# Kernel optimization log

Hardware: AMD Instinct MI355X
Metric: run time of the kernel (lower is better)

The kernel has to match this reference:

```python
import jax, jax.numpy as jnp
import numpy as np

B, S, D = 4, 2048, 512
H, DK, DV = 8, 64, 64

def setup_inputs() -> dict:
    key = jax.random.key(0)
    ks = jax.random.split(key, 11)
    s = 0.02
    return {
        "q_in": jax.random.normal(ks[0], (B, S, D), jnp.float32),
        "k_in": jax.random.normal(ks[1], (B, S, D), jnp.float32),
        "v_in": jax.random.normal(ks[2], (B, S, D), jnp.float32),
        "Wq": jax.random.normal(ks[3], (H, D, DK), jnp.float32) * s,
        "bq": jax.random.normal(ks[4], (H, DK), jnp.float32) * s,
        "Wk": jax.random.normal(ks[5], (H, D, DK), jnp.float32) * s,
        "bk": jax.random.normal(ks[6], (H, DK), jnp.float32) * s,
        "Wv": jax.random.normal(ks[7], (H, D, DV), jnp.float32) * s,
        "bv": jax.random.normal(ks[8], (H, DV), jnp.float32) * s,
        "Wo": jax.random.normal(ks[9], (H * DV, D), jnp.float32) * s,
        "bo": jax.random.normal(ks[10], (D,), jnp.float32) * s,
    }


def reference(q_in, k_in, v_in, Wq, bq, Wk, bk, Wv, bv, Wo, bo):
    # Per-head Q/K/V projections, batched over heads (same math as the
    # original Python loop over SingleAttention heads).
    q = jnp.einsum("bsd,hdk->bhsk", q_in, Wq) + bq[None, :, None, :]   # [B,H,S,DK]
    k = jnp.einsum("bsd,hdk->bhsk", k_in, Wk) + bk[None, :, None, :]   # [B,H,S,DK]
    v = jnp.einsum("bsd,hdv->bhsv", v_in, Wv) + bv[None, :, None, :]   # [B,H,S,DV]
    scale = 1.0 / jnp.sqrt(jnp.float32(DK))
    scores = jnp.einsum("bhqk,bhsk->bhqs", q, k) * scale               # [B,H,S,S]
    attn = jax.nn.softmax(scores, axis=-1)
    out = jnp.einsum("bhqs,bhsv->bhqv", attn, v)                        # [B,H,S,DV]
    # concat heads along feature dim: [B,S,H*DV]
    concat = out.transpose(0, 2, 1, 3).reshape(B, S, H * DV)
    return concat @ Wo + bo                                             # [B,S,D]
```

## Files before the change

### kernel.cpp

```cpp
#include <hip/hip_runtime.h>
#include <hip/hip_bf16.h>

using bf16 = __hip_bfloat16;
typedef short short8  __attribute__((ext_vector_type(8)));
typedef short short4v __attribute__((ext_vector_type(4)));
typedef float float4v __attribute__((ext_vector_type(4)));
typedef float f32x16  __attribute__((ext_vector_type(16)));
typedef unsigned int uint4v __attribute__((ext_vector_type(4)));

#define MFMA_BF16   __builtin_amdgcn_mfma_f32_16x16x32_bf16
#define MFMA32_BF16 __builtin_amdgcn_mfma_f32_32x32x16_bf16

#define B_  4
#define S_  2048
#define D_  512
#define H_  8
#define DK_ 64

__device__ __forceinline__ short f2bf(float f) {
  bf16 h = __float2bfloat16(f);
  return *reinterpret_cast<short*>(&h);
}

__device__ __forceinline__ unsigned cvtpk(float lo, float hi) {
  unsigned r;
  asm("v_cvt_pk_bf16_f32 %0, %1, %2" : "=v"(r) : "v"(lo), "v"(hi));
  return r;
}

__device__ __forceinline__ void plswap(unsigned& a, unsigned& b) {
  asm("v_permlane32_swap_b32 %0, %1" : "+v"(a), "+v"(b));
}

__device__ __forceinline__ short8 mk8(unsigned v0, unsigned v1, unsigned v2,
                                      unsigned v3) {
  uint4v u;
  u[0] = v0; u[1] = v1; u[2] = v2; u[3] = v3;
  return __builtin_bit_cast(short8, u);
}

#define GLL(g, l) __builtin_amdgcn_global_load_lds(                        \
      (const __attribute__((address_space(1))) void*)(g),                  \
      (__attribute__((address_space(3))) void*)(l), 16, 0, 0)

__global__ __launch_bounds__(256)
void prep(const float* __restrict__ qin, const float* __restrict__ kin,
          const float* __restrict__ vin, short* __restrict__ Xb,
          const float* __restrict__ Wq, const float* __restrict__ Wk,
          const float* __restrict__ Wv, const float* __restrict__ Wo,
          short* __restrict__ WqT, short* __restrict__ WkT,
          short* __restrict__ WvT, short* __restrict__ WoT) {
  __shared__ float tile[64 * 65];
  const int bid = blockIdx.x, tid = threadIdx.x;
  const size_t NTOK = (size_t)B_ * S_ * D_;

  if (bid < 6144) {
    const int z = bid >> 11, blk = bid & 2047;
    const float* src = (z == 0) ? qin : (z == 1) ? kin : vin;
    short* dst = Xb + (size_t)z * NTOK;
    const size_t base = ((size_t)blk * 256 + tid) * 8;
    float4v f0 = *(const float4v*)&src[base];
    float4v f1 = *(const float4v*)&src[base + 4];
    short8 s;
#pragma unroll
    for (int j = 0; j < 4; j++) { s[j] = f2bf(f0[j]); s[j + 4] = f2bf(f1[j]); }
    *(short8*)&dst[base] = s;
    return;
  }

  const int tw = bid - 6144;
  const int mat = tw >> 6, t = tw & 63;
  const float* W = (mat == 0) ? Wq : (mat == 1) ? Wk : (mat == 2) ? Wv : Wo;
  short* T       = (mat == 0) ? WqT : (mat == 1) ? WkT : (mat == 2) ? WvT : WoT;

  size_t sbase, ss, dbase;
  if (mat < 3) {
    int hh = t >> 3, d0 = (t & 7) * 64;
    sbase = (size_t)hh * 32768 + (size_t)d0 * 64;
    ss = 64;
    dbase = (size_t)hh * 64 * 512 + d0;
  } else {
    int n0 = (t >> 3) * 64, k0 = (t & 7) * 64;
    sbase = (size_t)k0 * 512 + n0;
    ss = 512;
    dbase = (size_t)n0 * 512 + k0;
  }

  {
    int r = tid >> 2, c0 = (tid & 3) * 16;
#pragma unroll
    for (int j = 0; j < 4; j++)
      *(float4v*)&tile[r * 65 + c0 + j * 4] =
          *(const float4v*)&W[sbase + (size_t)r * ss + c0 + j * 4];
  }
  __syncthreads();
  {
    int c = tid >> 2, r0 = (tid & 3) * 16;
#pragma unroll
    for (int j = 0; j < 2; j++) {
      short8 s;
#pragma unroll
      for (int u = 0; u < 8; u++) s[u] = f2bf(tile[(r0 + j * 8 + u) * 65 + c]);
      *(short8*)&T[dbase + (size_t)c * 512 + r0 + j * 8] = s;
    }
  }
}

__device__ __forceinline__ void gemm_core2(const short* __restrict__ A,
                                           const short* __restrict__ Bt,
                                           int m0, int n0,
                                           short* As, short* Bs,
                                           float4v acc[4][4]) {
  const int tid  = threadIdx.x;
  const int lane = tid & 63, wave = tid >> 6;
  const int quad = lane >> 4, l16 = lane & 15;
  const int wm = (wave >> 1) * 64, wn = (wave & 1) * 64;

  const int slot = wave * 256 + lane;

  for (int k0 = 0; k0 < 512; k0 += 64) {
    __syncthreads();
#pragma unroll
    for (int i = 0; i < 4; i++) {
      int s = slot + i * 64;
      int row = s >> 3, c8 = (s & 7) * 8;
      GLL(&A[(size_t)(m0 + row) * 512 + k0 + c8],
          &As[(size_t)(wave * 256 + i * 64) * 8]);
      GLL(&Bt[(size_t)(n0 + row) * 512 + k0 + c8],
          &Bs[(size_t)(wave * 256 + i * 64) * 8]);
    }
    __syncthreads();
#pragma unroll
    for (int ks = 0; ks < 64; ks += 32) {
      short8 af[4], bfr[4];
#pragma unroll
      for (int mi = 0; mi < 4; mi++)
        af[mi] = *(short8*)&As[(wm + mi * 16 + l16) * 64 + ks + quad * 8];
#pragma unroll
      for (int ni = 0; ni < 4; ni++)
        bfr[ni] = *(short8*)&Bs[(wn + ni * 16 + l16) * 64 + ks + quad * 8];
#pragma unroll
      for (int mi = 0; mi < 4; mi++)
#pragma unroll
        for (int ni = 0; ni < 4; ni++)
          acc[mi][ni] = MFMA_BF16(af[mi], bfr[ni], acc[mi][ni], 0, 0, 0);
    }
  }
}

__global__ __launch_bounds__(256, 2)
void qkv_gemm(const short* __restrict__ Xb,
              const short* __restrict__ WqT, const short* __restrict__ WkT,
              const short* __restrict__ WvT,
              const float* __restrict__ bq, const float* __restrict__ bk,
              const float* __restrict__ bv,
              short* __restrict__ Qp, short* __restrict__ Kp,
              short* __restrict__ Vt) {
  __shared__ __align__(16) short As[128 * 64];
  __shared__ __align__(16) short Bs[128 * 64];
  const int m0 = blockIdx.x * 128, n0 = blockIdx.y * 128;
  const int z = blockIdx.z;
  const size_t NTOK = (size_t)B_ * S_ * D_;
  const short* A    = Xb + (size_t)z * NTOK;
  const short* Bt   = (z == 0) ? WqT : (z == 1) ? WkT : WvT;
  const float* bias = (z == 0) ? bq  : (z == 1) ? bk  : bv;
  const float scale = (z == 0) ? 0.125f * 1.44269504088896f : 1.0f;

  float4v acc[4][4];
#pragma unroll
  for (int mi = 0; mi < 4; mi++)
#pragma unroll
    for (int ni = 0; ni < 4; ni++) acc[mi][ni] = (float4v){0.f, 0.f, 0.f, 0.f};

  gemm_core2(A, Bt, m0, n0, As, Bs, acc);

  const int lane = threadIdx.x & 63, wave = threadIdx.x >> 6;
  const int quad = lane >> 4, l16 = lane & 15;
  const int wm = (wave >> 1) * 64, wn = (wave & 1) * 64;

  if (z < 2) {
    short* out = (z == 0) ? Qp : Kp;
#pragma unroll
    for (int mi = 0; mi < 4; mi++) {
      int m = m0 + wm + mi * 16 + quad * 4;
      int b = m >> 11, s = m & 2047;
#pragma unroll
      for (int ni = 0; ni < 4; ni++) {
        int n = n0 + wn + ni * 16 + l16;
        int h = n >> 6, dk = n & 63;
        float bb = bias[n];
        size_t base = (((size_t)b * H_ + h) * S_ + s) * 64 + dk;
#pragma unroll
        for (int r = 0; r < 4; r++)
          out[base + (size_t)r * 64] = f2bf((acc[mi][ni][r] + bb) * scale);
      }
    }
  } else {
#pragma unroll
    for (int mi = 0; mi < 4; mi++) {
      int m = m0 + wm + mi * 16 + quad * 4;
      int b = m >> 11, s = m & 2047;
#pragma unroll
      for (int ni = 0; ni < 4; ni++) {
        int n = n0 + wn + ni * 16 + l16;
        int h = n >> 6, v = n & 63;
        float bb = bias[n];
        short4v pk;
#pragma unroll
        for (int r = 0; r < 4; r++) pk[r] = f2bf(acc[mi][ni][r] + bb);
        *(short4v*)&Vt[(((size_t)b * H_ + h) * 64 + v) * S_ + s] = pk;
      }
    }
  }
}

__global__ __launch_bounds__(256, 4)
void attn_kernel(const short* __restrict__ Qp, const short* __restrict__ Kp,
                 const short* __restrict__ Vt, short* __restrict__ Ao) {
  __shared__ __align__(16) short Ksh[2][4096];
  __shared__ __align__(16) short Vsh[2][4096];

  const int orig = blockIdx.y * gridDim.x + blockIdx.x;
  const int lb = (orig & 7) * 64 + (orig >> 3);
  const int qt = lb & 15, bh = lb >> 4;
  const int b = bh >> 3, h = bh & 7;

  const int tid = threadIdx.x;
  const int lane = tid & 63, wave = tid >> 6;
  const int l31 = lane & 31, hi = lane >> 5, s7 = l31 & 7;

  const short* Qb = Qp + (size_t)bh * S_ * 64;
  const short* Kb = Kp + (size_t)bh * S_ * 64;
  const short* Vb = Vt + (size_t)bh * 64 * S_;

  short8 qf[4];
  {
    const short* qrow = Qb + (size_t)(qt * 128 + wave * 32 + l31) * 64;
#pragma unroll
    for (int w = 0; w < 4; w++)
      qf[w] = *(const short8*)&qrow[w * 16 + hi * 8];
  }

  const int slot0 = wave * 128 + lane;
  const int kr0 = slot0 >> 3, kc0 = slot0 & 7;
  const int kr1 = kr0 + 8;
  const short* kg0 = Kb + (size_t)kr0 * 64 + ((kc0 ^ (kr0 & 7)) << 3);
  const short* kg1 = Kb + (size_t)kr1 * 64 + ((kc0 ^ (kr1 & 7)) << 3);
  const short* vg0 = Vb + (size_t)kr0 * S_ + ((kc0 ^ (kr0 & 7)) << 3);
  const short* vg1 = Vb + (size_t)kr1 * S_ + ((kc0 ^ (kr1 & 7)) << 3);

  f32x16 acc0, acc1;
#pragma unroll
  for (int r = 0; r < 16; r++) { acc0[r] = 0.f; acc1[r] = 0.f; }
  float ls0 = 0.f, ls1 = 0.f;

  {
    short* kd = &Ksh[0][wave * 1024];
    short* vd = &Vsh[0][wave * 1024];
    GLL(kg0, kd); GLL(kg1, kd + 512);
    GLL(vg0, vd); GLL(vg1, vd + 512);
  }
  __syncthreads();

  for (int t = 0; t < 32; t++) {
    const int cur = t & 1;
    if (t < 31) {
      short* kd = &Ksh[cur ^ 1][wave * 1024];
      short* vd = &Vsh[cur ^ 1][wave * 1024];
      GLL(kg0 + (size_t)(t + 1) * 4096, kd);
      GLL(kg1 + (size_t)(t + 1) * 4096, kd + 512);
      GLL(vg0 + (size_t)(t + 1) * 64, vd);
      GLL(vg1 + (size_t)(t + 1) * 64, vd + 512);
    }
    const short* kb = Ksh[cur];
    const short* vs = Vsh[cur];

#pragma unroll
    for (int kt = 0; kt < 2; kt++) {
      f32x16 sa;
#pragma unroll
      for (int r = 0; r < 16; r++) sa[r] = 0.f;
      __builtin_amdgcn_s_setprio(1);
#pragma unroll
      for (int w = 0; w < 4; w++) {
        short8 kf = *(const short8*)&kb[(kt * 32 + l31) * 64 +
                                        (((2 * w + hi) ^ s7) << 3)];
        sa = MFMA32_BF16(kf, qf[w], sa, 0, 0, 0);
      }
      __builtin_amdgcn_s_setprio(0);

      float pv[16];
#pragma unroll
      for (int r = 0; r < 16; r++) pv[r] = exp2f(sa[r]);
#pragma unroll
      for (int r = 0; r < 8; r++) { ls0 += pv[r]; ls1 += pv[r + 8]; }

      unsigned a0 = cvtpk(pv[0], pv[1]),  b0 = cvtpk(pv[4], pv[5]);
      plswap(a0, b0);
      unsigned c0 = cvtpk(pv[2], pv[3]),  d0 = cvtpk(pv[6], pv[7]);
      plswap(c0, d0);
      short8 pa0 = mk8(a0, c0, b0, d0);
      unsigned a1 = cvtpk(pv[8], pv[9]),  b1 = cvtpk(pv[12], pv[13]);
      plswap(a1, b1);
      unsigned c1 = cvtpk(pv[10], pv[11]), d1 = cvtpk(pv[14], pv[15]);
      plswap(c1, d1);
      short8 pa1 = mk8(a1, c1, b1, d1);

      __builtin_amdgcn_s_setprio(1);
      {
        const int kw0 = kt * 2, kw1 = kt * 2 + 1;
        short8 v00 = *(const short8*)&vs[l31 * 64 + (((2 * kw0 + hi) ^ s7) << 3)];
        short8 v10 = *(const short8*)&vs[(32 + l31) * 64 + (((2 * kw0 + hi) ^ s7) << 3)];
        acc0 = MFMA32_BF16(pa0, v00, acc0, 0, 0, 0);
        acc1 = MFMA32_BF16(pa0, v10, acc1, 0, 0, 0);
        short8 v01 = *(const short8*)&vs[l31 * 64 + (((2 * kw1 + hi) ^ s7) << 3)];
        short8 v11 = *(const short8*)&vs[(32 + l31) * 64 + (((2 * kw1 + hi) ^ s7) << 3)];
        acc0 = MFMA32_BF16(pa1, v01, acc0, 0, 0, 0);
        acc1 = MFMA32_BF16(pa1, v11, acc1, 0, 0, 0);
      }
      __builtin_amdgcn_s_setprio(0);
    }
    __syncthreads();
  }

  float lsum = ls0 + ls1;
  lsum += __shfl_xor(lsum, 32, 64);
  float myrl = 1.0f / lsum;

  const size_t obase =
      ((size_t)b * S_ + (size_t)(qt * 128 + wave * 32)) * D_ + h * 64 + l31;
#pragma unroll
  for (int r = 0; r < 16; r++) {
    int q = (r & 3) + 8 * (r >> 2) + 4 * hi;
    float rl = __shfl(myrl, q, 64);
    Ao[obase + (size_t)q * D_]      = f2bf(acc0[r] * rl);
    Ao[obase + (size_t)q * D_ + 32] = f2bf(acc1[r] * rl);
  }
}

__global__ __launch_bounds__(256, 2)
void out_gemm(const short* __restrict__ A, const short* __restrict__ Bt,
              const float* __restrict__ bias, float* __restrict__ out) {
  __shared__ __align__(16) short As[128 * 64];
  __shared__ __align__(16) short Bs[128 * 64];
  const int m0 = blockIdx.x * 128, n0 = blockIdx.y * 128;

  float4v acc[4][4];
#pragma unroll
  for (int mi = 0; mi < 4; mi++)
#pragma unroll
    for (int ni = 0; ni < 4; ni++) acc[mi][ni] = (float4v){0.f, 0.f, 0.f, 0.f};

  gemm_core2(A, Bt, m0, n0, As, Bs, acc);

  const int lane = threadIdx.x & 63, wave = threadIdx.x >> 6;
  const int quad = lane >> 4, l16 = lane & 15;
  const int wm = (wave >> 1) * 64, wn = (wave & 1) * 64;
#pragma unroll
  for (int mi = 0; mi < 4; mi++) {
    int m = m0 + wm + mi * 16 + quad * 4;
#pragma unroll
    for (int ni = 0; ni < 4; ni++) {
      int n = n0 + wn + ni * 16 + l16;
      float bb = bias[n];
#pragma unroll
      for (int r = 0; r < 4; r++)
        out[(size_t)(m + r) * 512 + n] = acc[mi][ni][r] + bb;
    }
  }
}

extern "C" void kernel_launch(void* const* d_in, const int* in_sizes, int n_in,
                              void* d_out, int out_size, void* d_ws, size_t ws_size,
                              hipStream_t stream) {
  const float* qin = (const float*)d_in[0];
  const float* kin = (const float*)d_in[1];
  const float* vin = (const float*)d_in[2];
  const float* Wq  = (const float*)d_in[3];
  const float* bq  = (const float*)d_in[4];
  const float* Wk  = (const float*)d_in[5];
  const float* bk  = (const float*)d_in[6];
  const float* Wv  = (const float*)d_in[7];
  const float* bv  = (const float*)d_in[8];
  const float* Wo  = (const float*)d_in[9];
  const float* bo  = (const float*)d_in[10];
  float* out = (float*)d_out;
  short* ws  = (short*)d_ws;

  const size_t NTOK = (size_t)B_ * S_ * D_;
  short* Qp  = ws;
  short* Kp  = ws + NTOK;
  short* Vt  = ws + 2 * NTOK;
  short* Ao  = ws + 3 * NTOK;
  short* WqT = ws + 4 * NTOK;
  short* WkT = WqT + 512 * 512;
  short* WvT = WkT + 512 * 512;
  short* WoT = WvT + 512 * 512;
  short* Xb  = WoT + 512 * 512;

  prep<<<dim3(6400), 256, 0, stream>>>(qin, kin, vin, Xb, Wq, Wk, Wv, Wo,
                                       WqT, WkT, WvT, WoT);
  qkv_gemm<<<dim3(64, 4, 3), 256, 0, stream>>>(Xb, WqT, WkT, WvT,
                                               bq, bk, bv, Qp, Kp, Vt);
  attn_kernel<<<dim3(16, 32), 256, 0, stream>>>(Qp, Kp, Vt, Ao);
  out_gemm<<<dim3(64, 4), 256, 0, stream>>>(Ao, WoT, bo, out);
}
```

Measured before the change: 205.4 us.

## Split attention KV range across two wave groups and swizzle GEMM LDS tiles

The attention kernel now launches 512 threads per block. Two groups of four waves each process half of the key/value sequence for the same query tile, then combine their partial accumulators and row sums through shared memory before the final normalization. This doubles the waves available to hide latency and halves the serial loop length, but adds an LDS reduction step and uses more shared memory per block. Separately, the GEMM core applies an XOR swizzle to its LDS tile layout to reduce bank conflicts on the fragment reads.

```diff
diff --git a/kernel.cpp b/kernel.cpp
--- a/kernel.cpp
+++ b/kernel.cpp
@@ -116,29 +116,33 @@
   const int quad = lane >> 4, l16 = lane & 15;
   const int wm = (wave >> 1) * 64, wn = (wave & 1) * 64;
 
-  const int slot = wave * 256 + lane;
-
   for (int k0 = 0; k0 < 512; k0 += 64) {
     __syncthreads();
 #pragma unroll
     for (int i = 0; i < 4; i++) {
-      int s = slot + i * 64;
-      int row = s >> 3, c8 = (s & 7) * 8;
-      GLL(&A[(size_t)(m0 + row) * 512 + k0 + c8],
+      int s = wave * 256 + i * 64 + lane;
+      int row = s >> 3, cs = s & 7;
+      int gc = (cs ^ (row & 7)) << 3;
+      GLL(&A[(size_t)(m0 + row) * 512 + k0 + gc],
           &As[(size_t)(wave * 256 + i * 64) * 8]);
-      GLL(&Bt[(size_t)(n0 + row) * 512 + k0 + c8],
+      GLL(&Bt[(size_t)(n0 + row) * 512 + k0 + gc],
           &Bs[(size_t)(wave * 256 + i * 64) * 8]);
     }
     __syncthreads();
 #pragma unroll
     for (int ks = 0; ks < 64; ks += 32) {
+      const int sr = (ks >> 3) + quad;
       short8 af[4], bfr[4];
 #pragma unroll
-      for (int mi = 0; mi < 4; mi++)
-        af[mi] = *(short8*)&As[(wm + mi * 16 + l16) * 64 + ks + quad * 8];
-#pragma unroll
-      for (int ni = 0; ni < 4; ni++)
-        bfr[ni] = *(short8*)&Bs[(wn + ni * 16 + l16) * 64 + ks + quad * 8];
+      for (int mi = 0; mi < 4; mi++) {
+        int row = wm + mi * 16 + l16;
+        af[mi] = *(short8*)&As[row * 64 + ((sr ^ (row & 7)) << 3)];
+      }
+#pragma unroll
+      for (int ni = 0; ni < 4; ni++) {
+        int row = wn + ni * 16 + l16;
+        bfr[ni] = *(short8*)&Bs[row * 64 + ((sr ^ (row & 7)) << 3)];
+      }
 #pragma unroll
       for (int mi = 0; mi < 4; mi++)
 #pragma unroll
@@ -214,11 +218,10 @@
   }
 }
 
-__global__ __launch_bounds__(256, 4)
+__global__ __launch_bounds__(512, 4)
 void attn_kernel(const short* __restrict__ Qp, const short* __restrict__ Kp,
                  const short* __restrict__ Vt, short* __restrict__ Ao) {
-  __shared__ __align__(16) short Ksh[2][4096];
-  __shared__ __align__(16) short Vsh[2][4096];
+  __shared__ __align__(16) short sh[32768];
 
   const int orig = blockIdx.y * gridDim.x + blockIdx.x;
   const int lb = (orig & 7) * 64 + (orig >> 3);
@@ -227,27 +230,31 @@
 
   const int tid = threadIdx.x;
   const int lane = tid & 63, wave = tid >> 6;
+  const int wg = wave & 3, half = wave >> 2;
   const int l31 = lane & 31, hi = lane >> 5, s7 = l31 & 7;
 
   const short* Qb = Qp + (size_t)bh * S_ * 64;
-  const short* Kb = Kp + (size_t)bh * S_ * 64;
+  const short* Kb = Kp + (size_t)bh * S_ * 64 + (size_t)half * 1024 * 64;
   const short* Vb = Vt + (size_t)bh * 64 * S_;
 
   short8 qf[4];
   {
-    const short* qrow = Qb + (size_t)(qt * 128 + wave * 32 + l31) * 64;
+    const short* qrow = Qb + (size_t)(qt * 128 + wg * 32 + l31) * 64;
 #pragma unroll
     for (int w = 0; w < 4; w++)
       qf[w] = *(const short8*)&qrow[w * 16 + hi * 8];
   }
 
-  const int slot0 = wave * 128 + lane;
+  const int slot0 = wg * 128 + lane;
   const int kr0 = slot0 >> 3, kc0 = slot0 & 7;
   const int kr1 = kr0 + 8;
   const short* kg0 = Kb + (size_t)kr0 * 64 + ((kc0 ^ (kr0 & 7)) << 3);
   const short* kg1 = Kb + (size_t)kr1 * 64 + ((kc0 ^ (kr1 & 7)) << 3);
-  const short* vg0 = Vb + (size_t)kr0 * S_ + ((kc0 ^ (kr0 & 7)) << 3);
-  const short* vg1 = Vb + (size_t)kr1 * S_ + ((kc0 ^ (kr1 & 7)) << 3);
+  const short* vg0 = Vb + (size_t)kr0 * S_ + half * 1024 + ((kc0 ^ (kr0 & 7)) << 3);
+  const short* vg1 = Vb + (size_t)kr1 * S_ + half * 1024 + ((kc0 ^ (kr1 & 7)) << 3);
+
+  short* Kbase = sh;
+  short* Vbase = sh + 16384;
 
   f32x16 acc0, acc1;
 #pragma unroll
@@ -255,25 +262,25 @@
   float ls0 = 0.f, ls1 = 0.f;
 
   {
-    short* kd = &Ksh[0][wave * 1024];
-    short* vd = &Vsh[0][wave * 1024];
+    short* kd = Kbase + (half * 2) * 4096 + wg * 1024;
+    short* vd = Vbase + (half * 2) * 4096 + wg * 1024;
     GLL(kg0, kd); GLL(kg1, kd + 512);
     GLL(vg0, vd); GLL(vg1, vd + 512);
   }
   __syncthreads();
 
-  for (int t = 0; t < 32; t++) {
+  for (int t = 0; t < 16; t++) {
     const int cur = t & 1;
-    if (t < 31) {
-      short* kd = &Ksh[cur ^ 1][wave * 1024];
-      short* vd = &Vsh[cur ^ 1][wave * 1024];
+    if (t < 15) {
+      short* kd = Kbase + (half * 2 + (cur ^ 1)) * 4096 + wg * 1024;
+      short* vd = Vbase + (half * 2 + (cur ^ 1)) * 4096 + wg * 1024;
       GLL(kg0 + (size_t)(t + 1) * 4096, kd);
       GLL(kg1 + (size_t)(t + 1) * 4096, kd + 512);
       GLL(vg0 + (size_t)(t + 1) * 64, vd);
       GLL(vg1 + (size_t)(t + 1) * 64, vd + 512);
     }
-    const short* kb = Ksh[cur];
-    const short* vs = Vsh[cur];
+    const short* kb = Kbase + (half * 2 + cur) * 4096;
+    const short* vs = Vbase + (half * 2 + cur) * 4096;
 
 #pragma unroll
     for (int kt = 0; kt < 2; kt++) {
@@ -325,10 +332,39 @@
 
   float lsum = ls0 + ls1;
   lsum += __shfl_xor(lsum, 32, 64);
+
+  float* fsh = (float*)sh;
+  if (half == 1) {
+    const int base = wg * 2304 + lane * 36;
+#pragma unroll
+    for (int r = 0; r < 16; r += 4) {
+      *(float4v*)&fsh[base + r] =
+          (float4v){acc0[r], acc0[r + 1], acc0[r + 2], acc0[r + 3]};
+      *(float4v*)&fsh[base + 16 + r] =
+          (float4v){acc1[r], acc1[r + 1], acc1[r + 2], acc1[r + 3]};
+    }
+    if (lane < 32) fsh[9216 + wg * 32 + l31] = lsum;
+  }
+  __syncthreads();
+  if (half == 1) return;
+
+  {
+    const int base = wg * 2304 + lane * 36;
+#pragma unroll
+    for (int r = 0; r < 16; r += 4) {
+      float4v u0 = *(float4v*)&fsh[base + r];
+      acc0[r] += u0[0]; acc0[r + 1] += u0[1];
+      acc0[r + 2] += u0[2]; acc0[r + 3] += u0[3];
+      float4v u1 = *(float4v*)&fsh[base + 16 + r];
+      acc1[r] += u1[0]; acc1[r + 1] += u1[1];
+      acc1[r + 2] += u1[2]; acc1[r + 3] += u1[3];
+    }
+    lsum += fsh[9216 + wg * 32 + l31];
+  }
   float myrl = 1.0f / lsum;
 
   const size_t obase =
-      ((size_t)b * S_ + (size_t)(qt * 128 + wave * 32)) * D_ + h * 64 + l31;
+      ((size_t)b * S_ + (size_t)(qt * 128 + wg * 32)) * D_ + h * 64 + l31;
 #pragma unroll
   for (int r = 0; r < 16; r++) {
     int q = (r & 3) + 8 * (r >> 2) + 4 * hi;
@@ -402,6 +438,6 @@
                                        WqT, WkT, WvT, WoT);
   qkv_gemm<<<dim3(64, 4, 3), 256, 0, stream>>>(Xb, WqT, WkT, WvT,
                                                bq, bk, bv, Qp, Kp, Vt);
-  attn_kernel<<<dim3(16, 32), 256, 0, stream>>>(Qp, Kp, Vt, Ao);
+  attn_kernel<<<dim3(16, 32), 512, 0, stream>>>(Qp, Kp, Vt, Ao);
   out_gemm<<<dim3(64, 4), 256, 0, stream>>>(Ao, WoT, bo, out);
 }
```

Measured after the change: 196.5 us. 1.04x faster.
